# Performance work log

Measured on AMD Instinct MI355X. Metric: run time of the kernel, lower is better.

## Reference

```python
import jax, jax.numpy as jnp
import numpy as np

BS, H, W, C = 32, 64, 64, 256
SEQ = 32


def setup_inputs() -> dict:
    key = jax.random.key(0)
    k1, k2, k3, k4, k5 = jax.random.split(key, 5)
    x = jax.random.normal(k1, (BS, H, W, C), dtype=jnp.float32)
    sentence = jax.random.normal(k2, (BS, C), dtype=jnp.float32)  # unused in call()
    context = jax.random.normal(k3, (BS, SEQ, C), dtype=jnp.float32)
    mask = jax.random.bernoulli(k4, 0.3, (BS, SEQ))
    W_word = jax.random.normal(k5, (C, C), dtype=jnp.float32) * (1.0 / np.sqrt(C))
    return {"x": x, "sentence": sentence, "context": context, "mask": mask, "W_word": W_word}


def reference(x, sentence, context, mask, W_word):
    bs, h, w, c = x.shape
    hw = h * w
    seq = context.shape[1]
    xf = x.reshape(bs, hw, c)                                   # [bs, hw, C]
    ctx = jnp.einsum('bsd,dc->bsc', context, W_word)            # conv1x1 word projection
    attn = jnp.einsum('bnc,bsc->bns', xf, ctx)                  # [bs, hw, seq]
    attn = attn.reshape(bs * hw, seq)
    # faithful to original: mask tiled hw times along axis 0 (block-repeat order)
    mask_t = jnp.tile(mask, (hw, 1))                            # [bs*hw, seq]
    neg_inf = jnp.asarray(-jnp.inf, dtype=attn.dtype)
    attn = jnp.where(mask_t, neg_inf, attn)
    attn = jax.nn.softmax(attn, axis=-1).reshape(bs, hw, seq)
    # matmul(ctx^T, attn^T) -> [bs, C, hw] -> transpose -> [bs, hw, C]
    weighted_context = jnp.einsum('bsc,bns->bnc', ctx, attn).reshape(bs, h, w, c)
    word_attn = attn.reshape(bs, h, w, seq)
    return weighted_context, word_attn
```

## Files before the change

kernel.cpp:

```cpp
#include <hip/hip_runtime.h>
#include <stdint.h>

typedef __attribute__((ext_vector_type(8))) short short8;
typedef __attribute__((ext_vector_type(4))) float float4v;

#define HW   4096
#define CC   256
#define SEQQ 32
#define BSZ  32
#define ROWS 64

#define SGRP     1032
#define CTXT_SZ  (8 * SGRP)
#define PSTR_P   40

static __device__ __forceinline__ uint16_t f2bf(float f) {
  union { float f; uint32_t u; } v; v.f = f;
  uint32_t r = v.u + 0x7FFFu + ((v.u >> 16) & 1u);
  return (uint16_t)(r >> 16);
}
static __device__ __forceinline__ float bf2f(uint16_t h) {
  union { uint32_t u; float f; } v; v.u = ((uint32_t)h) << 16;
  return v.f;
}

extern "C" __global__ __launch_bounds__(256) void prep_kernel(
    const float* __restrict__ ctx_in,
    const float* __restrict__ Wp,
    const void*  __restrict__ mask,
    uint32_t* __restrict__ maskbits_ws,
    uint16_t* __restrict__ hiT_ws,
    uint16_t* __restrict__ loT_ws)
{
  const int t = threadIdx.x;
  if (blockIdx.x == 256) {
    __shared__ int byteFlag;
    if (t == 0) byteFlag = 0;
    __syncthreads();
    const uint8_t* mb = (const uint8_t*)mask;
    int nz = 0;
    for (int i = t; i < 1024; i += 256)
      if ((i & 3) == 1 && mb[i] != 0) nz = 1;
    if (nz) atomicOr(&byteFlag, 1);
    __syncthreads();
    const bool byteMode = (byteFlag != 0);
    const uint32_t* mw32 = (const uint32_t*)mask;
    if (t < 32) {
      uint32_t bits = 0;
      for (int s = 0; s < 32; ++s) {
        bool m = byteMode ? (mb[t * 32 + s] != 0) : (mw32[t * 32 + s] != 0);
        if (m) bits |= (1u << s);
      }
      maskbits_ws[t] = bits;
    }
    return;
  }

  const int r0 = blockIdx.x * 4;
  __shared__ float crow[4][CC];
  for (int i = t; i < 1024; i += 256)
    crow[i >> 8][i & 255] = ctx_in[(size_t)r0 * CC + i];
  __syncthreads();

  const int j  = t >> 6;
  const int c4 = (t & 63) << 2;
  float4v acc = {0.f, 0.f, 0.f, 0.f};
  #pragma unroll 8
  for (int d = 0; d < CC; ++d) {
    float s = crow[j][d];
    const float4 wv = *(const float4*)&Wp[(size_t)d * CC + c4];
    acc[0] += s * wv.x; acc[1] += s * wv.y;
    acc[2] += s * wv.z; acc[3] += s * wv.w;
  }

  const int row = r0 + j, bb = row >> 5, ss = row & 31;
  const size_t base = (size_t)bb * CTXT_SZ + (ss >> 2) * SGRP + (ss & 3) * 16;
  #pragma unroll
  for (int q = 0; q < 4; ++q) {
    const int c = c4 + q;
    const float v = acc[q];
    const uint16_t h  = f2bf(v);
    const uint16_t lo = f2bf(v - bf2f(h));
    const size_t idx = base + (c >> 4) * 64 + (c & 15);
    hiT_ws[idx] = h;
    loT_ws[idx] = lo;
  }
}

extern "C" __global__ __launch_bounds__(256, 4) void attn_main(
    const float* __restrict__ x,
    const uint8_t* __restrict__ ws,
    float* __restrict__ out0,
    float* __restrict__ out1)
{
  const uint32_t* maskbits_ws = (const uint32_t*)ws;
  const uint16_t* hiT_ws = (const uint16_t*)(ws + 128);
  const uint16_t* loT_ws = hiT_ws + (size_t)BSZ * CTXT_SZ;

  __shared__ __align__(16) uint16_t hiT[CTXT_SZ];
  __shared__ __align__(16) uint16_t loT[CTXT_SZ];
  __shared__ __align__(16) uint16_t pL[ROWS * PSTR_P];
  __shared__ uint32_t maskW[32];

  const int tid = threadIdx.x;
  const int b   = blockIdx.y;
  const int n0  = blockIdx.x * ROWS;

  {
    const uint4* sHi = (const uint4*)(hiT_ws + (size_t)b * CTXT_SZ);
    const uint4* sLo = (const uint4*)(loT_ws + (size_t)b * CTXT_SZ);
    uint4* dHi = (uint4*)hiT;
    uint4* dLo = (uint4*)loT;
    #pragma unroll
    for (int k = 0; k < 4; ++k) {
      dHi[tid + k * 256] = sHi[tid + k * 256];
      dLo[tid + k * 256] = sLo[tid + k * 256];
    }
    if (tid < 8) { dHi[1024 + tid] = sHi[1024 + tid]; dLo[1024 + tid] = sLo[1024 + tid]; }
    if (tid < 32) maskW[tid] = maskbits_ws[tid];
  }
  __syncthreads();

  const int w    = tid >> 6;
  const int lane = tid & 63;
  const int l15  = lane & 15;
  const int quad = lane >> 4;
  const int nbase = n0 + w * 16;

  float4v acc0 = {0.f, 0.f, 0.f, 0.f};
  float4v acc1 = {0.f, 0.f, 0.f, 0.f};
  const float* xrow = x + ((size_t)b * HW + nbase + l15) * CC + quad * 8;
  const int sbase = (l15 >> 2) * SGRP + (l15 & 3) * 16 + (quad >> 1) * 64 + (quad & 1) * 8;

  for (int k0 = 0; k0 < 8; ++k0) {
    float4 xa = *(const float4*)(xrow + k0 * 32);
    float4 xb = *(const float4*)(xrow + k0 * 32 + 4);
    float xv[8] = {xa.x, xa.y, xa.z, xa.w, xb.x, xb.y, xb.z, xb.w};
    short8 ah, al;
    #pragma unroll
    for (int jj = 0; jj < 8; ++jj) {
      uint32_t u = __float_as_uint(xv[jj]);
      ah[jj] = (short)(u >> 16);
      float r = xv[jj] - __uint_as_float(u & 0xFFFF0000u);
      al[jj] = (short)(__float_as_uint(r) >> 16);
    }
    const int ka = sbase + k0 * 128;
    short8 bh0 = *(const short8*)&hiT[ka];
    short8 bl0 = *(const short8*)&loT[ka];
    short8 bh1 = *(const short8*)&hiT[ka + 4 * SGRP];
    short8 bl1 = *(const short8*)&loT[ka + 4 * SGRP];
    acc0 = __builtin_amdgcn_mfma_f32_16x16x32_bf16(ah, bh0, acc0, 0, 0, 0);
    acc0 = __builtin_amdgcn_mfma_f32_16x16x32_bf16(ah, bl0, acc0, 0, 0, 0);
    acc0 = __builtin_amdgcn_mfma_f32_16x16x32_bf16(al, bh0, acc0, 0, 0, 0);
    acc1 = __builtin_amdgcn_mfma_f32_16x16x32_bf16(ah, bh1, acc1, 0, 0, 0);
    acc1 = __builtin_amdgcn_mfma_f32_16x16x32_bf16(ah, bl1, acc1, 0, 0, 0);
    acc1 = __builtin_amdgcn_mfma_f32_16x16x32_bf16(al, bh1, acc1, 0, 0, 0);
  }

  #pragma unroll
  for (int r = 0; r < 4; ++r) {
    const int n = nbase + quad * 4 + r;
    const uint32_t mwd = maskW[n & 31];
    float v0 = (mwd & (1u << l15))        ? -1e30f : acc0[r];
    float v1 = (mwd & (1u << (l15 + 16))) ? -1e30f : acc1[r];
    float mx = fmaxf(v0, v1);
    #pragma unroll
    for (int off = 1; off < 16; off <<= 1)
      mx = fmaxf(mx, __shfl_xor(mx, off, 64));
    float e0 = __expf(v0 - mx);
    float e1 = __expf(v1 - mx);
    float sm = e0 + e1;
    #pragma unroll
    for (int off = 1; off < 16; off <<= 1)
      sm += __shfl_xor(sm, off, 64);
    float inv = 1.0f / sm;
    float p0 = e0 * inv, p1 = e1 * inv;
    size_t o1 = ((size_t)b * HW + n) * SEQQ;
    out1[o1 + l15]      = p0;
    out1[o1 + 16 + l15] = p1;
    pL[(w * 16 + quad * 4 + r) * PSTR_P + l15]      = f2bf(p0);
    pL[(w * 16 + quad * 4 + r) * PSTR_P + 16 + l15] = f2bf(p1);
  }

  short8 pa = *(const short8*)&pL[(w * 16 + l15) * PSTR_P + quad * 8];
  const int cbase = quad * 2 * SGRP + l15;
  #pragma unroll
  for (int ct = 0; ct < 16; ++ct) {
    short8 bfr;
    #pragma unroll
    for (int jj = 0; jj < 8; ++jj)
      bfr[jj] = (short)hiT[cbase + (jj >> 2) * SGRP + ct * 64 + (jj & 3) * 16];
    float4v z = {0.f, 0.f, 0.f, 0.f};
    float4v d = __builtin_amdgcn_mfma_f32_16x16x32_bf16(pa, bfr, z, 0, 0, 0);
    #pragma unroll
    for (int r = 0; r < 4; ++r) {
      size_t o0 = ((size_t)b * HW + nbase + quad * 4 + r) * CC + ct * 16 + l15;
      out0[o0] = d[r];
    }
  }
}

extern "C" void kernel_launch(void* const* d_in, const int* in_sizes, int n_in,
                              void* d_out, int out_size, void* d_ws, size_t ws_size,
                              hipStream_t stream) {
  const float* x      = (const float*)d_in[0];
  const float* ctx_in = (const float*)d_in[2];
  const void*  mask   = d_in[3];
  const float* Wp     = (const float*)d_in[4];

  float* out0 = (float*)d_out;
  float* out1 = out0 + (size_t)BSZ * HW * CC;

  uint8_t*  ws          = (uint8_t*)d_ws;
  uint32_t* maskbits_ws = (uint32_t*)ws;
  uint16_t* hiT_ws      = (uint16_t*)(ws + 128);
  uint16_t* loT_ws      = hiT_ws + (size_t)BSZ * CTXT_SZ;

  prep_kernel<<<257, 256, 0, stream>>>(ctx_in, Wp, mask, maskbits_ws,
                                       hiT_ws, loT_ws);
  attn_main<<<dim3(HW / ROWS, BSZ), 256, 0, stream>>>(x, ws, out0, out1);
}
```

Baseline: 289.7 us.

## Transpose MFMA operands for row-per-lane softmax and vectorized output stores

Swaps the A/B operands of both MFMA stages so that each lane holds four consecutive columns of one row. The outputs can then be written as float4 stores instead of scalar strided stores, and the softmax reduces in-register with only two cross-lane shuffles. It also preloads all x tiles up front and relaxes the launch bound from 4 to 2 blocks per SM, which raises the register budget at the cost of occupancy.

```diff
diff --git a/kernel.cpp b/kernel.cpp
--- a/kernel.cpp
+++ b/kernel.cpp
@@ -87,7 +87,7 @@
   }
 }
 
-extern "C" __global__ __launch_bounds__(256, 4) void attn_main(
+extern "C" __global__ __launch_bounds__(256, 2) void attn_main(
     const float* __restrict__ x,
     const uint8_t* __restrict__ ws,
     float* __restrict__ out0,
@@ -132,10 +132,17 @@
   const float* xrow = x + ((size_t)b * HW + nbase + l15) * CC + quad * 8;
   const int sbase = (l15 >> 2) * SGRP + (l15 & 3) * 16 + (quad >> 1) * 64 + (quad & 1) * 8;
 
+  float4 xa[8], xb[8];
+  #pragma unroll
   for (int k0 = 0; k0 < 8; ++k0) {
-    float4 xa = *(const float4*)(xrow + k0 * 32);
-    float4 xb = *(const float4*)(xrow + k0 * 32 + 4);
-    float xv[8] = {xa.x, xa.y, xa.z, xa.w, xb.x, xb.y, xb.z, xb.w};
+    xa[k0] = *(const float4*)(xrow + k0 * 32);
+    xb[k0] = *(const float4*)(xrow + k0 * 32 + 4);
+  }
+
+  #pragma unroll
+  for (int k0 = 0; k0 < 8; ++k0) {
+    float xv[8] = {xa[k0].x, xa[k0].y, xa[k0].z, xa[k0].w,
+                   xb[k0].x, xb[k0].y, xb[k0].z, xb[k0].w};
     short8 ah, al;
     #pragma unroll
     for (int jj = 0; jj < 8; ++jj) {
@@ -149,41 +156,54 @@
     short8 bl0 = *(const short8*)&loT[ka];
     short8 bh1 = *(const short8*)&hiT[ka + 4 * SGRP];
     short8 bl1 = *(const short8*)&loT[ka + 4 * SGRP];
-    acc0 = __builtin_amdgcn_mfma_f32_16x16x32_bf16(ah, bh0, acc0, 0, 0, 0);
-    acc0 = __builtin_amdgcn_mfma_f32_16x16x32_bf16(ah, bl0, acc0, 0, 0, 0);
-    acc0 = __builtin_amdgcn_mfma_f32_16x16x32_bf16(al, bh0, acc0, 0, 0, 0);
-    acc1 = __builtin_amdgcn_mfma_f32_16x16x32_bf16(ah, bh1, acc1, 0, 0, 0);
-    acc1 = __builtin_amdgcn_mfma_f32_16x16x32_bf16(ah, bl1, acc1, 0, 0, 0);
-    acc1 = __builtin_amdgcn_mfma_f32_16x16x32_bf16(al, bh1, acc1, 0, 0, 0);
-  }
-
-  #pragma unroll
-  for (int r = 0; r < 4; ++r) {
-    const int n = nbase + quad * 4 + r;
+    acc0 = __builtin_amdgcn_mfma_f32_16x16x32_bf16(bh0, ah, acc0, 0, 0, 0);
+    acc0 = __builtin_amdgcn_mfma_f32_16x16x32_bf16(bl0, ah, acc0, 0, 0, 0);
+    acc0 = __builtin_amdgcn_mfma_f32_16x16x32_bf16(bh0, al, acc0, 0, 0, 0);
+    acc1 = __builtin_amdgcn_mfma_f32_16x16x32_bf16(bh1, ah, acc1, 0, 0, 0);
+    acc1 = __builtin_amdgcn_mfma_f32_16x16x32_bf16(bl1, ah, acc1, 0, 0, 0);
+    acc1 = __builtin_amdgcn_mfma_f32_16x16x32_bf16(bh1, al, acc1, 0, 0, 0);
+  }
+
+  {
+    const int n = nbase + l15;
     const uint32_t mwd = maskW[n & 31];
-    float v0 = (mwd & (1u << l15))        ? -1e30f : acc0[r];
-    float v1 = (mwd & (1u << (l15 + 16))) ? -1e30f : acc1[r];
-    float mx = fmaxf(v0, v1);
-    #pragma unroll
-    for (int off = 1; off < 16; off <<= 1)
-      mx = fmaxf(mx, __shfl_xor(mx, off, 64));
-    float e0 = __expf(v0 - mx);
-    float e1 = __expf(v1 - mx);
-    float sm = e0 + e1;
-    #pragma unroll
-    for (int off = 1; off < 16; off <<= 1)
-      sm += __shfl_xor(sm, off, 64);
-    float inv = 1.0f / sm;
-    float p0 = e0 * inv, p1 = e1 * inv;
-    size_t o1 = ((size_t)b * HW + n) * SEQQ;
-    out1[o1 + l15]      = p0;
-    out1[o1 + 16 + l15] = p1;
-    pL[(w * 16 + quad * 4 + r) * PSTR_P + l15]      = f2bf(p0);
-    pL[(w * 16 + quad * 4 + r) * PSTR_P + 16 + l15] = f2bf(p1);
+    float v[8];
+    #pragma unroll
+    for (int r = 0; r < 4; ++r) {
+      v[r]     = (mwd & (1u << (quad * 4 + r)))      ? -1e30f : acc0[r];
+      v[4 + r] = (mwd & (1u << (16 + quad * 4 + r))) ? -1e30f : acc1[r];
+    }
+    float mx = v[0];
+    #pragma unroll
+    for (int j = 1; j < 8; ++j) mx = fmaxf(mx, v[j]);
+    mx = fmaxf(mx, __shfl_xor(mx, 16, 64));
+    mx = fmaxf(mx, __shfl_xor(mx, 32, 64));
+    float e[8], sm = 0.f;
+    #pragma unroll
+    for (int j = 0; j < 8; ++j) { e[j] = __expf(v[j] - mx); sm += e[j]; }
+    sm += __shfl_xor(sm, 16, 64);
+    sm += __shfl_xor(sm, 32, 64);
+    const float inv = 1.0f / sm;
+    float p[8];
+    #pragma unroll
+    for (int j = 0; j < 8; ++j) p[j] = e[j] * inv;
+
+    float* o1row = out1 + ((size_t)b * HW + n) * SEQQ;
+    *(float4*)(o1row + quad * 4)      = make_float4(p[0], p[1], p[2], p[3]);
+    *(float4*)(o1row + 16 + quad * 4) = make_float4(p[4], p[5], p[6], p[7]);
+
+    uint32_t w0 = (uint32_t)f2bf(p[0]) | ((uint32_t)f2bf(p[1]) << 16);
+    uint32_t w1 = (uint32_t)f2bf(p[2]) | ((uint32_t)f2bf(p[3]) << 16);
+    uint32_t w2 = (uint32_t)f2bf(p[4]) | ((uint32_t)f2bf(p[5]) << 16);
+    uint32_t w3 = (uint32_t)f2bf(p[6]) | ((uint32_t)f2bf(p[7]) << 16);
+    uint16_t* prow = &pL[(w * 16 + l15) * PSTR_P];
+    *(uint2*)(prow + quad * 4)      = make_uint2(w0, w1);
+    *(uint2*)(prow + 16 + quad * 4) = make_uint2(w2, w3);
   }
 
   short8 pa = *(const short8*)&pL[(w * 16 + l15) * PSTR_P + quad * 8];
   const int cbase = quad * 2 * SGRP + l15;
+  float* orow = out0 + ((size_t)b * HW + nbase + l15) * CC;
   #pragma unroll
   for (int ct = 0; ct < 16; ++ct) {
     short8 bfr;
@@ -191,12 +211,8 @@
     for (int jj = 0; jj < 8; ++jj)
       bfr[jj] = (short)hiT[cbase + (jj >> 2) * SGRP + ct * 64 + (jj & 3) * 16];
     float4v z = {0.f, 0.f, 0.f, 0.f};
-    float4v d = __builtin_amdgcn_mfma_f32_16x16x32_bf16(pa, bfr, z, 0, 0, 0);
-    #pragma unroll
-    for (int r = 0; r < 4; ++r) {
-      size_t o0 = ((size_t)b * HW + nbase + quad * 4 + r) * CC + ct * 16 + l15;
-      out0[o0] = d[r];
-    }
+    float4v d = __builtin_amdgcn_mfma_f32_16x16x32_bf16(bfr, pa, z, 0, 0, 0);
+    *(float4*)(orow + ct * 16 + quad * 4) = make_float4(d[0], d[1], d[2], d[3]);
   }
 }
 
```

After: 291.8 us. About the same (+0.8%).

## Process two row tiles per wave with prefetched x and vectorized stores

Applied to the files above, without the earlier changes.

Each block now handles 128 rows, with each wave doing two 16-row tiles. This halves how often the per-batch context tables are loaded into shared memory. The x loads for the first tile are issued before the shared-memory fill, and the second tile's loads before compute, to overlap global latency. The MFMA operands are swapped so each lane owns a full output row, which allows float4 stores to both outputs and a simpler softmax reduction. The cost is more registers, fewer resident blocks (launch bounds 2), and half as many blocks in the grid.

```diff
diff --git a/kernel.cpp b/kernel.cpp
--- a/kernel.cpp
+++ b/kernel.cpp
@@ -8,7 +8,7 @@
 #define CC   256
 #define SEQQ 32
 #define BSZ  32
-#define ROWS 64
+#define RPB  128
 
 #define SGRP     1032
 #define CTXT_SZ  (8 * SGRP)
@@ -87,7 +87,81 @@
   }
 }
 
-extern "C" __global__ __launch_bounds__(256, 4) void attn_main(
+#define COMPUTE_TILE(XA, XB, TBASE)                                           \
+  {                                                                           \
+    float4v acc0 = {0.f, 0.f, 0.f, 0.f};                                      \
+    float4v acc1 = {0.f, 0.f, 0.f, 0.f};                                      \
+    _Pragma("unroll")                                                         \
+    for (int k0 = 0; k0 < 8; ++k0) {                                          \
+      float xv[8] = {XA[k0].x, XA[k0].y, XA[k0].z, XA[k0].w,                  \
+                     XB[k0].x, XB[k0].y, XB[k0].z, XB[k0].w};                 \
+      short8 ah, al;                                                          \
+      _Pragma("unroll")                                                       \
+      for (int jj = 0; jj < 8; ++jj) {                                        \
+        uint32_t u = __float_as_uint(xv[jj]);                                 \
+        ah[jj] = (short)(u >> 16);                                            \
+        float rr = xv[jj] - __uint_as_float(u & 0xFFFF0000u);                 \
+        al[jj] = (short)(__float_as_uint(rr) >> 16);                          \
+      }                                                                       \
+      const int ka = sbase + k0 * 128;                                        \
+      short8 bh0 = *(const short8*)&hiT[ka];                                  \
+      short8 bl0 = *(const short8*)&loT[ka];                                  \
+      short8 bh1 = *(const short8*)&hiT[ka + 4 * SGRP];                       \
+      short8 bl1 = *(const short8*)&loT[ka + 4 * SGRP];                       \
+      acc0 = __builtin_amdgcn_mfma_f32_16x16x32_bf16(bh0, ah, acc0, 0, 0, 0); \
+      acc0 = __builtin_amdgcn_mfma_f32_16x16x32_bf16(bl0, ah, acc0, 0, 0, 0); \
+      acc0 = __builtin_amdgcn_mfma_f32_16x16x32_bf16(bh0, al, acc0, 0, 0, 0); \
+      acc1 = __builtin_amdgcn_mfma_f32_16x16x32_bf16(bh1, ah, acc1, 0, 0, 0); \
+      acc1 = __builtin_amdgcn_mfma_f32_16x16x32_bf16(bl1, ah, acc1, 0, 0, 0); \
+      acc1 = __builtin_amdgcn_mfma_f32_16x16x32_bf16(bh1, al, acc1, 0, 0, 0); \
+    }                                                                         \
+    const int n = (TBASE) + l15;                                              \
+    const uint32_t mwd = maskW[n & 31];                                       \
+    float v[8];                                                               \
+    _Pragma("unroll")                                                         \
+    for (int r = 0; r < 4; ++r) {                                             \
+      v[r]     = (mwd & (1u << (quad * 4 + r)))      ? -1e30f : acc0[r];      \
+      v[4 + r] = (mwd & (1u << (16 + quad * 4 + r))) ? -1e30f : acc1[r];      \
+    }                                                                         \
+    float mx = v[0];                                                          \
+    _Pragma("unroll")                                                         \
+    for (int jq = 1; jq < 8; ++jq) mx = fmaxf(mx, v[jq]);                     \
+    mx = fmaxf(mx, __shfl_xor(mx, 16, 64));                                   \
+    mx = fmaxf(mx, __shfl_xor(mx, 32, 64));                                   \
+    float e[8], sm = 0.f;                                                     \
+    _Pragma("unroll")                                                         \
+    for (int jq = 0; jq < 8; ++jq) { e[jq] = __expf(v[jq] - mx); sm += e[jq]; } \
+    sm += __shfl_xor(sm, 16, 64);                                             \
+    sm += __shfl_xor(sm, 32, 64);                                             \
+    const float inv = 1.0f / sm;                                              \
+    float p[8];                                                               \
+    _Pragma("unroll")                                                         \
+    for (int jq = 0; jq < 8; ++jq) p[jq] = e[jq] * inv;                       \
+    float* o1row = out1 + ((size_t)b * HW + n) * SEQQ;                        \
+    *(float4*)(o1row + quad * 4)      = make_float4(p[0], p[1], p[2], p[3]);  \
+    *(float4*)(o1row + 16 + quad * 4) = make_float4(p[4], p[5], p[6], p[7]);  \
+    uint32_t w0 = (uint32_t)f2bf(p[0]) | ((uint32_t)f2bf(p[1]) << 16);        \
+    uint32_t w1 = (uint32_t)f2bf(p[2]) | ((uint32_t)f2bf(p[3]) << 16);        \
+    uint32_t w2 = (uint32_t)f2bf(p[4]) | ((uint32_t)f2bf(p[5]) << 16);        \
+    uint32_t w3 = (uint32_t)f2bf(p[6]) | ((uint32_t)f2bf(p[7]) << 16);        \
+    uint16_t* prow = &pL[(w * 16 + l15) * PSTR_P];                            \
+    *(uint2*)(prow + quad * 4)      = make_uint2(w0, w1);                     \
+    *(uint2*)(prow + 16 + quad * 4) = make_uint2(w2, w3);                     \
+    short8 pa = *(const short8*)&pL[(w * 16 + l15) * PSTR_P + quad * 8];      \
+    float* orow = out0 + ((size_t)b * HW + n) * CC;                           \
+    _Pragma("unroll")                                                         \
+    for (int ct = 0; ct < 16; ++ct) {                                         \
+      short8 bfr;                                                             \
+      _Pragma("unroll")                                                       \
+      for (int jj = 0; jj < 8; ++jj)                                          \
+        bfr[jj] = (short)hiT[cbase + (jj >> 2) * SGRP + ct * 64 + (jj & 3) * 16]; \
+      float4v z = {0.f, 0.f, 0.f, 0.f};                                       \
+      float4v d = __builtin_amdgcn_mfma_f32_16x16x32_bf16(bfr, pa, z, 0, 0, 0); \
+      *(float4*)(orow + ct * 16 + quad * 4) = make_float4(d[0], d[1], d[2], d[3]); \
+    }                                                                         \
+  }
+
+extern "C" __global__ __launch_bounds__(256, 2) void attn_main(
     const float* __restrict__ x,
     const uint8_t* __restrict__ ws,
     float* __restrict__ out0,
@@ -99,105 +173,65 @@
 
   __shared__ __align__(16) uint16_t hiT[CTXT_SZ];
   __shared__ __align__(16) uint16_t loT[CTXT_SZ];
-  __shared__ __align__(16) uint16_t pL[ROWS * PSTR_P];
+  __shared__ __align__(16) uint16_t pL[64 * PSTR_P];
   __shared__ uint32_t maskW[32];
 
   const int tid = threadIdx.x;
   const int b   = blockIdx.y;
-  const int n0  = blockIdx.x * ROWS;
+  const int n0  = blockIdx.x * RPB;
+
+  const int w    = tid >> 6;
+  const int lane = tid & 63;
+  const int l15  = lane & 15;
+  const int quad = lane >> 4;
+  const int nwave = n0 + w * 32;
+
+  const uint4* sHi = (const uint4*)(hiT_ws + (size_t)b * CTXT_SZ);
+  const uint4* sLo = (const uint4*)(loT_ws + (size_t)b * CTXT_SZ);
+
+  uint4 hS[4], lS[4];
+  #pragma unroll
+  for (int k = 0; k < 4; ++k) {
+    hS[k] = sHi[tid + k * 256];
+    lS[k] = sLo[tid + k * 256];
+  }
+
+  const float* xrow0 = x + ((size_t)b * HW + nwave + l15) * CC + quad * 8;
+  float4 xa0[8], xb0[8];
+  #pragma unroll
+  for (int k0 = 0; k0 < 8; ++k0) {
+    xa0[k0] = *(const float4*)(xrow0 + k0 * 32);
+    xb0[k0] = *(const float4*)(xrow0 + k0 * 32 + 4);
+  }
+  asm volatile("" ::: "memory");
 
   {
-    const uint4* sHi = (const uint4*)(hiT_ws + (size_t)b * CTXT_SZ);
-    const uint4* sLo = (const uint4*)(loT_ws + (size_t)b * CTXT_SZ);
     uint4* dHi = (uint4*)hiT;
     uint4* dLo = (uint4*)loT;
     #pragma unroll
     for (int k = 0; k < 4; ++k) {
-      dHi[tid + k * 256] = sHi[tid + k * 256];
-      dLo[tid + k * 256] = sLo[tid + k * 256];
+      dHi[tid + k * 256] = hS[k];
+      dLo[tid + k * 256] = lS[k];
     }
     if (tid < 8) { dHi[1024 + tid] = sHi[1024 + tid]; dLo[1024 + tid] = sLo[1024 + tid]; }
     if (tid < 32) maskW[tid] = maskbits_ws[tid];
   }
   __syncthreads();
 
-  const int w    = tid >> 6;
-  const int lane = tid & 63;
-  const int l15  = lane & 15;
-  const int quad = lane >> 4;
-  const int nbase = n0 + w * 16;
-
-  float4v acc0 = {0.f, 0.f, 0.f, 0.f};
-  float4v acc1 = {0.f, 0.f, 0.f, 0.f};
-  const float* xrow = x + ((size_t)b * HW + nbase + l15) * CC + quad * 8;
+  const float* xrow1 = xrow0 + 16 * CC;
+  float4 xa1[8], xb1[8];
+  #pragma unroll
+  for (int k0 = 0; k0 < 8; ++k0) {
+    xa1[k0] = *(const float4*)(xrow1 + k0 * 32);
+    xb1[k0] = *(const float4*)(xrow1 + k0 * 32 + 4);
+  }
+  asm volatile("" ::: "memory");
+
   const int sbase = (l15 >> 2) * SGRP + (l15 & 3) * 16 + (quad >> 1) * 64 + (quad & 1) * 8;
-
-  for (int k0 = 0; k0 < 8; ++k0) {
-    float4 xa = *(const float4*)(xrow + k0 * 32);
-    float4 xb = *(const float4*)(xrow + k0 * 32 + 4);
-    float xv[8] = {xa.x, xa.y, xa.z, xa.w, xb.x, xb.y, xb.z, xb.w};
-    short8 ah, al;
-    #pragma unroll
-    for (int jj = 0; jj < 8; ++jj) {
-      uint32_t u = __float_as_uint(xv[jj]);
-      ah[jj] = (short)(u >> 16);
-      float r = xv[jj] - __uint_as_float(u & 0xFFFF0000u);
-      al[jj] = (short)(__float_as_uint(r) >> 16);
-    }
-    const int ka = sbase + k0 * 128;
-    short8 bh0 = *(const short8*)&hiT[ka];
-    short8 bl0 = *(const short8*)&loT[ka];
-    short8 bh1 = *(const short8*)&hiT[ka + 4 * SGRP];
-    short8 bl1 = *(const short8*)&loT[ka + 4 * SGRP];
-    acc0 = __builtin_amdgcn_mfma_f32_16x16x32_bf16(ah, bh0, acc0, 0, 0, 0);
-    acc0 = __builtin_amdgcn_mfma_f32_16x16x32_bf16(ah, bl0, acc0, 0, 0, 0);
-    acc0 = __builtin_amdgcn_mfma_f32_16x16x32_bf16(al, bh0, acc0, 0, 0, 0);
-    acc1 = __builtin_amdgcn_mfma_f32_16x16x32_bf16(ah, bh1, acc1, 0, 0, 0);
-    acc1 = __builtin_amdgcn_mfma_f32_16x16x32_bf16(ah, bl1, acc1, 0, 0, 0);
-    acc1 = __builtin_amdgcn_mfma_f32_16x16x32_bf16(al, bh1, acc1, 0, 0, 0);
-  }
-
-  #pragma unroll
-  for (int r = 0; r < 4; ++r) {
-    const int n = nbase + quad * 4 + r;
-    const uint32_t mwd = maskW[n & 31];
-    float v0 = (mwd & (1u << l15))        ? -1e30f : acc0[r];
-    float v1 = (mwd & (1u << (l15 + 16))) ? -1e30f : acc1[r];
-    float mx = fmaxf(v0, v1);
-    #pragma unroll
-    for (int off = 1; off < 16; off <<= 1)
-      mx = fmaxf(mx, __shfl_xor(mx, off, 64));
-    float e0 = __expf(v0 - mx);
-    float e1 = __expf(v1 - mx);
-    float sm = e0 + e1;
-    #pragma unroll
-    for (int off = 1; off < 16; off <<= 1)
-      sm += __shfl_xor(sm, off, 64);
-    float inv = 1.0f / sm;
-    float p0 = e0 * inv, p1 = e1 * inv;
-    size_t o1 = ((size_t)b * HW + n) * SEQQ;
-    out1[o1 + l15]      = p0;
-    out1[o1 + 16 + l15] = p1;
-    pL[(w * 16 + quad * 4 + r) * PSTR_P + l15]      = f2bf(p0);
-    pL[(w * 16 + quad * 4 + r) * PSTR_P + 16 + l15] = f2bf(p1);
-  }
-
-  short8 pa = *(const short8*)&pL[(w * 16 + l15) * PSTR_P + quad * 8];
   const int cbase = quad * 2 * SGRP + l15;
-  #pragma unroll
-  for (int ct = 0; ct < 16; ++ct) {
-    short8 bfr;
-    #pragma unroll
-    for (int jj = 0; jj < 8; ++jj)
-      bfr[jj] = (short)hiT[cbase + (jj >> 2) * SGRP + ct * 64 + (jj & 3) * 16];
-    float4v z = {0.f, 0.f, 0.f, 0.f};
-    float4v d = __builtin_amdgcn_mfma_f32_16x16x32_bf16(pa, bfr, z, 0, 0, 0);
-    #pragma unroll
-    for (int r = 0; r < 4; ++r) {
-      size_t o0 = ((size_t)b * HW + nbase + quad * 4 + r) * CC + ct * 16 + l15;
-      out0[o0] = d[r];
-    }
-  }
+
+  COMPUTE_TILE(xa0, xb0, nwave);
+  COMPUTE_TILE(xa1, xb1, nwave + 16);
 }
 
 extern "C" void kernel_launch(void* const* d_in, const int* in_sizes, int n_in,
@@ -218,5 +252,5 @@
 
   prep_kernel<<<257, 256, 0, stream>>>(ctx_in, Wp, mask, maskbits_ws,
                                        hiT_ws, loT_ws);
-  attn_main<<<dim3(HW / ROWS, BSZ), 256, 0, stream>>>(x, ws, out0, out1);
-}
+  attn_main<<<dim3(HW / RPB, BSZ), 256, 0, stream>>>(x, ws, out0, out1);
+}
```

Result: no change. 284.2 us (-1.9%).
